# Performance work log

Measured on AMD Instinct MI355X. Metric: run time of the kernel, lower is better.

Reference implementation:

```python
import jax, jax.numpy as jnp
import numpy as np

STRIDE = 1
PAD = 1
K = 3  # kernel is asserted 3x3 in the original module


def _conv2d(x, w, b):
    out = jax.lax.conv_general_dilated(
        x, w, (STRIDE, STRIDE), [(PAD, PAD), (PAD, PAD)],
        dimension_numbers=("NCHW", "OIHW", "NCHW"))
    return out + b[None, :, None, None]


def _bilinear_sample(img, py, px):
    # img: [C, H, W]; py, px: [9, Ho, Wo] float sampling coords.
    # Zero-padded bilinear sampling (matches torchvision deform_conv2d).
    H, W = img.shape[1], img.shape[2]
    y0f = jnp.floor(py)
    x0f = jnp.floor(px)
    ly = py - y0f
    lx = px - x0f
    y0 = y0f.astype(jnp.int32)
    x0 = x0f.astype(jnp.int32)

    def g(yi, xi):
        valid = ((yi >= 0) & (yi < H) & (xi >= 0) & (xi < W)).astype(img.dtype)
        v = img[:, jnp.clip(yi, 0, H - 1), jnp.clip(xi, 0, W - 1)]  # [C,9,Ho,Wo]
        return v * valid[None]

    v00 = g(y0, x0)
    v01 = g(y0, x0 + 1)
    v10 = g(y0 + 1, x0)
    v11 = g(y0 + 1, x0 + 1)
    return (v00 * (1 - ly) * (1 - lx) + v01 * (1 - ly) * lx
            + v10 * ly * (1 - lx) + v11 * ly * lx)  # [C,9,Ho,Wo]


def setup_inputs() -> dict:
    key = jax.random.key(0)
    k1, k2, k3, k4 = jax.random.split(key, 4)
    B, C_in, C_out, H, W = 8, 64, 64, 128, 128
    x = jax.random.normal(k1, (B, C_in, H, W), dtype=jnp.float32)
    # offset predictor params (zero-init in original; small random here so
    # offsets are non-trivial, ~1-2 px)
    offset_w = jax.random.normal(k2, (4, C_in, K, K), dtype=jnp.float32) * 0.05
    offset_b = jax.random.normal(k3, (4,), dtype=jnp.float32) * 0.05
    weight = jax.random.normal(k4, (C_out, C_in, K, K), dtype=jnp.float32)
    return {"x": x, "offset_w": offset_w, "offset_b": offset_b, "weight": weight}


def reference(x, offset_w, offset_b, weight):
    B, C, H, W = x.shape
    o = _conv2d(x, offset_w, offset_b)  # [B, 4, Ho, Wo]
    o_t, o_b, o_l, o_r = o[:, 0], o[:, 1], o[:, 2], o[:, 3]
    z = jnp.zeros_like(o_t)
    # Original builds offset = cat([o_t,0,o_b]*3, [o_l]*3,[0]*3,[o_r]*3) (18 ch)
    # and torchvision reads interleaved (dy_k, dx_k) = (ch[2k], ch[2k+1]).
    # Faithful literal per-kernel-point offsets:
    dy = jnp.stack([o_t, o_b, z, o_t, o_b, o_l, z, z, o_r], axis=1)  # [B,9,Ho,Wo]
    dx = jnp.stack([z, o_t, o_b, z, o_l, o_l, z, o_r, o_r], axis=1)  # [B,9,Ho,Wo]
    Ho, Wo = o.shape[2], o.shape[3]
    ki = jnp.arange(9) // 3
    kj = jnp.arange(9) % 3
    base_y = (jnp.arange(Ho)[None, :, None] * STRIDE - PAD + ki[:, None, None])  # [9,Ho,1]
    base_x = (jnp.arange(Wo)[None, None, :] * STRIDE - PAD + kj[:, None, None])  # [9,1,Wo]
    py = base_y.astype(x.dtype) + dy  # [B,9,Ho,Wo]
    px = base_x.astype(x.dtype) + dx
    sampled = jax.vmap(_bilinear_sample)(x, py, px)  # [B,C,9,Ho,Wo]
    out = jnp.einsum("bckhw,ock->bohw", sampled,
                     weight.reshape(weight.shape[0], C, 9))
    return out
```

## Files before the change

### kernel.cpp

```cpp
#include <hip/hip_runtime.h>

#define H_   128
#define W_   128
#define CIN  64
#define COUT 64
#define B_   8
#define HW_  (H_*W_)

__global__ __launch_bounds__(256) void offsets_kernel(
    const float* __restrict__ x, const float* __restrict__ ow,
    const float* __restrict__ ob, float* __restrict__ o)
{
    __shared__ float xs[16][4][W_];
    __shared__ __align__(16) float wl[576][4];

    int tid = threadIdx.x;
    int blk = blockIdx.x;
    int b  = blk >> 6;
    int h0 = (blk & 63) << 1;

    for (int idx = tid; idx < 2304; idx += 256) {
        int ck = idx >> 2, j = idx & 3;
        int c = ck / 9, kk = ck - c * 9;
        wl[ck][j] = ow[(j * CIN + c) * 9 + kk];
    }

    float acc0 = 0.f, acc1 = 0.f, acc2 = 0.f, acc3 = 0.f;
    int hr = tid >> 7;
    int w  = tid & 127;

    for (int cc = 0; cc < 4; ++cc) {
        __syncthreads();
        for (int idx = tid; idx < 16 * 4 * W_; idx += 256) {
            int c_l = idx >> 9;
            int rem = idx & 511;
            int row = rem >> 7;
            int ww  = rem & 127;
            int gy  = h0 - 1 + row;
            float v = 0.f;
            if (gy >= 0 && gy < H_)
                v = x[((size_t)(b * CIN + cc * 16 + c_l) * H_ + gy) * W_ + ww];
            xs[c_l][row][ww] = v;
        }
        __syncthreads();
        for (int c_l = 0; c_l < 16; ++c_l) {
            int ckbase = (cc * 16 + c_l) * 9;
            #pragma unroll
            for (int ki = 0; ki < 3; ++ki) {
                #pragma unroll
                for (int kj = 0; kj < 3; ++kj) {
                    int wx = w - 1 + kj;
                    float v = (wx >= 0 && wx < W_) ? xs[c_l][hr + ki][wx] : 0.f;
                    float4 wv = *(const float4*)&wl[ckbase + ki * 3 + kj][0];
                    acc0 += v * wv.x; acc1 += v * wv.y;
                    acc2 += v * wv.z; acc3 += v * wv.w;
                }
            }
        }
    }

    int h = h0 + hr;
    size_t base = ((size_t)(b * 4) * H_ + h) * W_ + w;
    o[base]            = acc0 + ob[0];
    o[base + HW_]      = acc1 + ob[1];
    o[base + 2 * HW_]  = acc2 + ob[2];
    o[base + 3 * HW_]  = acc3 + ob[3];
}

__global__ void wtrans_kernel(const float* __restrict__ w, float* __restrict__ wT)
{
    int idx = blockIdx.x * 256 + threadIdx.x;
    if (idx < 576 * COUT) {
        int ck = idx >> 6, co = idx & 63;
        wT[idx] = w[co * 576 + ck];
    }
}

__global__ __launch_bounds__(256) void main_kernel(
    const float* __restrict__ x, const float* __restrict__ o,
    const float* __restrict__ wT, float* __restrict__ out)
{
    __shared__ __align__(16) int   aaddr[9][64][4];
    __shared__ __align__(16) float awt[9][64][4];
    __shared__ __align__(16) float s_lds[72 * 64];
    __shared__ __align__(16) float w_lds[72 * 64];

    int tid = threadIdx.x;
    int blk = blockIdx.x;
    int b   = blk >> 8;
    int rem = blk & 255;
    int h   = rem >> 1;
    int w0  = (rem & 1) << 6;

    for (int idx = tid; idx < 576; idx += 256) {
        int p = idx & 63;
        int k = idx >> 6;
        int w = w0 + p;
        size_t obase = ((size_t)(b * 4) * H_ + h) * W_ + w;
        float t  = o[obase];
        float bo = o[obase + HW_];
        float l  = o[obase + 2 * HW_];
        float r  = o[obase + 3 * HW_];
        float dy, dx;
        switch (k) {
            case 0: dy = t;   dx = 0.f; break;
            case 1: dy = bo;  dx = t;   break;
            case 2: dy = 0.f; dx = bo;  break;
            case 3: dy = t;   dx = 0.f; break;
            case 4: dy = bo;  dx = l;   break;
            case 5: dy = l;   dx = l;   break;
            case 6: dy = 0.f; dx = 0.f; break;
            case 7: dy = 0.f; dx = r;   break;
            default: dy = r;  dx = r;   break;
        }
        float py = (float)(h - 1 + k / 3) + dy;
        float px = (float)(w - 1 + (k % 3)) + dx;
        float y0f = floorf(py), x0f = floorf(px);
        float ly = py - y0f, lx = px - x0f;
        int y0 = (int)y0f, x0 = (int)x0f;
        int y1 = y0 + 1,   x1 = x0 + 1;
        bool vy0 = ((unsigned)y0 < (unsigned)H_);
        bool vy1 = ((unsigned)y1 < (unsigned)H_);
        bool vx0 = ((unsigned)x0 < (unsigned)W_);
        bool vx1 = ((unsigned)x1 < (unsigned)W_);
        int y0c = min(max(y0, 0), H_ - 1), y1c = min(max(y1, 0), H_ - 1);
        int x0c = min(max(x0, 0), W_ - 1), x1c = min(max(x1, 0), W_ - 1);
        aaddr[k][p][0] = y0c * W_ + x0c;
        aaddr[k][p][1] = y0c * W_ + x1c;
        aaddr[k][p][2] = y1c * W_ + x0c;
        aaddr[k][p][3] = y1c * W_ + x1c;
        float omly = 1.f - ly, omlx = 1.f - lx;
        awt[k][p][0] = (vy0 && vx0) ? omly * omlx : 0.f;
        awt[k][p][1] = (vy0 && vx1) ? omly * lx   : 0.f;
        awt[k][p][2] = (vy1 && vx0) ? ly * omlx   : 0.f;
        awt[k][p][3] = (vy1 && vx1) ? ly * lx     : 0.f;
    }
    __syncthreads();

    float acc[4][4] = {};
    int tp = tid & 15;
    int tc = tid >> 4;
    const float4* wT4 = (const float4*)wT;

    for (int cc = 0; cc < 8; ++cc) {
        for (int idx = tid; idx < 72 * 64; idx += 256) {
            int p = idx & 63;
            int r = idx >> 6;
            int k   = r % 9;
            int c_l = r / 9;
            int4   a4 = *(const int4*)&aaddr[k][p][0];
            float4 w4 = *(const float4*)&awt[k][p][0];
            const float* xb = x + ((size_t)(b * CIN + cc * 8 + c_l) << 14);
            float s = w4.x * xb[a4.x] + w4.y * xb[a4.y]
                    + w4.z * xb[a4.z] + w4.w * xb[a4.w];
            s_lds[idx] = s;
        }
        for (int idx = tid; idx < 1152; idx += 256) {
            ((float4*)w_lds)[idx] = wT4[cc * 1152 + idx];
        }
        __syncthreads();
        #pragma unroll 8
        for (int r = 0; r < 72; ++r) {
            float4 sv = *(const float4*)&s_lds[r * 64 + tp * 4];
            float4 wv = *(const float4*)&w_lds[r * 64 + tc * 4];
            float svv[4] = {sv.x, sv.y, sv.z, sv.w};
            float wvv[4] = {wv.x, wv.y, wv.z, wv.w};
            #pragma unroll
            for (int i = 0; i < 4; ++i)
                #pragma unroll
                for (int j = 0; j < 4; ++j)
                    acc[i][j] += svv[i] * wvv[j];
        }
        __syncthreads();
    }

    #pragma unroll
    for (int j = 0; j < 4; ++j) {
        int co = tc * 4 + j;
        size_t ob2 = ((size_t)(b * COUT + co) * H_ + h) * W_ + w0 + tp * 4;
        float4 v = make_float4(acc[0][j], acc[1][j], acc[2][j], acc[3][j]);
        *(float4*)&out[ob2] = v;
    }
}

extern "C" void kernel_launch(void* const* d_in, const int* in_sizes, int n_in,
                              void* d_out, int out_size, void* d_ws, size_t ws_size,
                              hipStream_t stream)
{
    const float* x  = (const float*)d_in[0];
    const float* ow = (const float*)d_in[1];
    const float* ob = (const float*)d_in[2];
    const float* wt = (const float*)d_in[3];
    float* out  = (float*)d_out;
    float* o_ws = (float*)d_ws;
    float* wT   = o_ws + (size_t)B_ * 4 * HW_;

    offsets_kernel<<<dim3(512), dim3(256), 0, stream>>>(x, ow, ob, o_ws);
    wtrans_kernel<<<dim3(144), dim3(256), 0, stream>>>(wt, wT);
    main_kernel<<<dim3(2048), dim3(256), 0, stream>>>(x, o_ws, wT, out);
}
```

Baseline: 434.4 us.

## Rewrite deformable conv main loop with bf16 MFMA and per-row blocks

Result: faster. 408.3 us (-6.0%).

```diff
diff --git a/kernel.cpp b/kernel.cpp
--- a/kernel.cpp
+++ b/kernel.cpp
@@ -7,116 +7,134 @@
 #define B_   8
 #define HW_  (H_*W_)
 
-__global__ __launch_bounds__(256) void offsets_kernel(
-    const float* __restrict__ x, const float* __restrict__ ow,
+typedef __attribute__((ext_vector_type(8))) short  short8;
+typedef __attribute__((ext_vector_type(8))) __bf16 bf16x8;
+typedef __attribute__((ext_vector_type(4))) float  f32x4;
+
+__device__ __forceinline__ ushort bf16r(float f) {
+    uint u = __builtin_bit_cast(uint, f);
+    u += 0x7fff + ((u >> 16) & 1);
+    return (ushort)(u >> 16);
+}
+
+__global__ void prep_kernel(const float* __restrict__ wt, const float* __restrict__ ow,
+                            float* __restrict__ owT, ushort* __restrict__ wTT2)
+{
+    int idx = blockIdx.x * 256 + threadIdx.x;
+    if (idx < 9 * 64 * 64) {
+        int kk = idx >> 12;
+        int r  = idx & 4095;
+        int co = r >> 6, c = r & 63;
+        wTT2[idx] = bf16r(wt[(co * 64 + c) * 9 + kk]);
+    }
+    if (idx < 576 * 4) {
+        int ck = idx >> 2, j = idx & 3;
+        owT[idx] = ow[j * 576 + ck];
+    }
+}
+
+__global__ __launch_bounds__(128) void offsets_kernel(
+    const float* __restrict__ x, const float* __restrict__ owT,
     const float* __restrict__ ob, float* __restrict__ o)
 {
-    __shared__ float xs[16][4][W_];
-    __shared__ __align__(16) float wl[576][4];
+    __shared__ float xs[16][3][132];
 
     int tid = threadIdx.x;
     int blk = blockIdx.x;
-    int b  = blk >> 6;
-    int h0 = (blk & 63) << 1;
-
-    for (int idx = tid; idx < 2304; idx += 256) {
-        int ck = idx >> 2, j = idx & 3;
-        int c = ck / 9, kk = ck - c * 9;
-        wl[ck][j] = ow[(j * CIN + c) * 9 + kk];
-    }
-
-    float acc0 = 0.f, acc1 = 0.f, acc2 = 0.f, acc3 = 0.f;
-    int hr = tid >> 7;
-    int w  = tid & 127;
+    int b = blk >> 7, h = blk & 127;
+    int w = tid;
+
+    for (int i = tid; i < 16 * 3; i += 128) {
+        int c = i / 3, r = i - c * 3;
+        xs[c][r][0] = 0.f; xs[c][r][1] = 0.f;
+        xs[c][r][130] = 0.f; xs[c][r][131] = 0.f;
+    }
+
+    float a0 = 0.f, a1 = 0.f, a2 = 0.f, a3 = 0.f;
+    const float4* owT4 = (const float4*)owT;
 
     for (int cc = 0; cc < 4; ++cc) {
         __syncthreads();
-        for (int idx = tid; idx < 16 * 4 * W_; idx += 256) {
-            int c_l = idx >> 9;
-            int rem = idx & 511;
-            int row = rem >> 7;
-            int ww  = rem & 127;
-            int gy  = h0 - 1 + row;
+        for (int idx = tid; idx < 16 * 3 * 128; idx += 128) {
+            int c_l = idx / 384;
+            int rem = idx - c_l * 384;
+            int row = rem >> 7, ww = rem & 127;
+            int gy = h - 1 + row;
             float v = 0.f;
-            if (gy >= 0 && gy < H_)
+            if ((unsigned)gy < (unsigned)H_)
                 v = x[((size_t)(b * CIN + cc * 16 + c_l) * H_ + gy) * W_ + ww];
-            xs[c_l][row][ww] = v;
-        }
-        __syncthreads();
+            xs[c_l][row][ww + 2] = v;
+        }
+        __syncthreads();
+        #pragma unroll
         for (int c_l = 0; c_l < 16; ++c_l) {
-            int ckbase = (cc * 16 + c_l) * 9;
+            int ckb = (cc * 16 + c_l) * 9;
             #pragma unroll
             for (int ki = 0; ki < 3; ++ki) {
                 #pragma unroll
                 for (int kj = 0; kj < 3; ++kj) {
-                    int wx = w - 1 + kj;
-                    float v = (wx >= 0 && wx < W_) ? xs[c_l][hr + ki][wx] : 0.f;
-                    float4 wv = *(const float4*)&wl[ckbase + ki * 3 + kj][0];
-                    acc0 += v * wv.x; acc1 += v * wv.y;
-                    acc2 += v * wv.z; acc3 += v * wv.w;
+                    float v = xs[c_l][ki][w + kj + 1];
+                    float4 wv = owT4[ckb + ki * 3 + kj];
+                    a0 += v * wv.x; a1 += v * wv.y;
+                    a2 += v * wv.z; a3 += v * wv.w;
                 }
             }
         }
     }
 
-    int h = h0 + hr;
     size_t base = ((size_t)(b * 4) * H_ + h) * W_ + w;
-    o[base]            = acc0 + ob[0];
-    o[base + HW_]      = acc1 + ob[1];
-    o[base + 2 * HW_]  = acc2 + ob[2];
-    o[base + 3 * HW_]  = acc3 + ob[3];
-}
-
-__global__ void wtrans_kernel(const float* __restrict__ w, float* __restrict__ wT)
-{
-    int idx = blockIdx.x * 256 + threadIdx.x;
-    if (idx < 576 * COUT) {
-        int ck = idx >> 6, co = idx & 63;
-        wT[idx] = w[co * 576 + ck];
-    }
-}
-
-__global__ __launch_bounds__(256) void main_kernel(
+    o[base]           = a0 + ob[0];
+    o[base + HW_]     = a1 + ob[1];
+    o[base + 2 * HW_] = a2 + ob[2];
+    o[base + 3 * HW_] = a3 + ob[3];
+}
+
+__global__ __launch_bounds__(128) void main_kernel(
     const float* __restrict__ x, const float* __restrict__ o,
-    const float* __restrict__ wT, float* __restrict__ out)
-{
-    __shared__ __align__(16) int   aaddr[9][64][4];
-    __shared__ __align__(16) float awt[9][64][4];
-    __shared__ __align__(16) float s_lds[72 * 64];
-    __shared__ __align__(16) float w_lds[72 * 64];
-
-    int tid = threadIdx.x;
-    int blk = blockIdx.x;
-    int b   = blk >> 8;
-    int rem = blk & 255;
-    int h   = rem >> 1;
-    int w0  = (rem & 1) << 6;
-
-    for (int idx = tid; idx < 576; idx += 256) {
-        int p = idx & 63;
-        int k = idx >> 6;
-        int w = w0 + p;
-        size_t obase = ((size_t)(b * 4) * H_ + h) * W_ + w;
-        float t  = o[obase];
-        float bo = o[obase + HW_];
-        float l  = o[obase + 2 * HW_];
-        float r  = o[obase + 3 * HW_];
+    const ushort* __restrict__ wTT2, float* __restrict__ out)
+{
+    __shared__ ushort a_lds[128][72];
+    __shared__ ushort w_lds[64][72];
+
+    int tid  = threadIdx.x;
+    int blk  = blockIdx.x;
+    int b    = blk >> 7, h = blk & 127;
+    int w    = tid;
+    int lane = tid & 63, wid = tid >> 6;
+
+    size_t obase = ((size_t)(b * 4) * H_ + h) * W_ + w;
+    float t  = o[obase];
+    float bo = o[obase + HW_];
+    float l_ = o[obase + 2 * HW_];
+    float r_ = o[obase + 3 * HW_];
+
+    const float* xb = x + ((size_t)b * CIN * HW_);
+
+    f32x4 zero4 = {0.f, 0.f, 0.f, 0.f};
+    f32x4 acc[4][4];
+    #pragma unroll
+    for (int i = 0; i < 4; ++i)
+        #pragma unroll
+        for (int j = 0; j < 4; ++j) acc[i][j] = zero4;
+
+    for (int cc = 0; cc < 9; ++cc) {
         float dy, dx;
-        switch (k) {
+        switch (cc) {
             case 0: dy = t;   dx = 0.f; break;
             case 1: dy = bo;  dx = t;   break;
             case 2: dy = 0.f; dx = bo;  break;
             case 3: dy = t;   dx = 0.f; break;
-            case 4: dy = bo;  dx = l;   break;
-            case 5: dy = l;   dx = l;   break;
+            case 4: dy = bo;  dx = l_;  break;
+            case 5: dy = l_;  dx = l_;  break;
             case 6: dy = 0.f; dx = 0.f; break;
-            case 7: dy = 0.f; dx = r;   break;
-            default: dy = r;  dx = r;   break;
-        }
-        float py = (float)(h - 1 + k / 3) + dy;
-        float px = (float)(w - 1 + (k % 3)) + dx;
-        float y0f = floorf(py), x0f = floorf(px);
-        float ly = py - y0f, lx = px - x0f;
+            case 7: dy = 0.f; dx = r_;  break;
+            default: dy = r_; dx = r_;  break;
+        }
+        int ki = cc / 3, kj = cc - ki * 3;
+        float py  = (float)(h - 1 + ki) + dy;
+        float pxf = (float)(w - 1 + kj) + dx;
+        float y0f = floorf(py), x0f = floorf(pxf);
+        float ly = py - y0f, lx = pxf - x0f;
         int y0 = (int)y0f, x0 = (int)x0f;
         int y1 = y0 + 1,   x1 = x0 + 1;
         bool vy0 = ((unsigned)y0 < (unsigned)H_);
@@ -125,61 +143,71 @@
         bool vx1 = ((unsigned)x1 < (unsigned)W_);
         int y0c = min(max(y0, 0), H_ - 1), y1c = min(max(y1, 0), H_ - 1);
         int x0c = min(max(x0, 0), W_ - 1), x1c = min(max(x1, 0), W_ - 1);
-        aaddr[k][p][0] = y0c * W_ + x0c;
-        aaddr[k][p][1] = y0c * W_ + x1c;
-        aaddr[k][p][2] = y1c * W_ + x0c;
-        aaddr[k][p][3] = y1c * W_ + x1c;
+        int ia0 = y0c * W_ + x0c, ia1 = y0c * W_ + x1c;
+        int ia2 = y1c * W_ + x0c, ia3 = y1c * W_ + x1c;
         float omly = 1.f - ly, omlx = 1.f - lx;
-        awt[k][p][0] = (vy0 && vx0) ? omly * omlx : 0.f;
-        awt[k][p][1] = (vy0 && vx1) ? omly * lx   : 0.f;
-        awt[k][p][2] = (vy1 && vx0) ? ly * omlx   : 0.f;
-        awt[k][p][3] = (vy1 && vx1) ? ly * lx     : 0.f;
-    }
-    __syncthreads();
-
-    float acc[4][4] = {};
-    int tp = tid & 15;
-    int tc = tid >> 4;
-    const float4* wT4 = (const float4*)wT;
-
-    for (int cc = 0; cc < 8; ++cc) {
-        for (int idx = tid; idx < 72 * 64; idx += 256) {
-            int p = idx & 63;
-            int r = idx >> 6;
-            int k   = r % 9;
-            int c_l = r / 9;
-            int4   a4 = *(const int4*)&aaddr[k][p][0];
-            float4 w4 = *(const float4*)&awt[k][p][0];
-            const float* xb = x + ((size_t)(b * CIN + cc * 8 + c_l) << 14);
-            float s = w4.x * xb[a4.x] + w4.y * xb[a4.y]
-                    + w4.z * xb[a4.z] + w4.w * xb[a4.w];
-            s_lds[idx] = s;
-        }
-        for (int idx = tid; idx < 1152; idx += 256) {
-            ((float4*)w_lds)[idx] = wT4[cc * 1152 + idx];
-        }
-        __syncthreads();
-        #pragma unroll 8
-        for (int r = 0; r < 72; ++r) {
-            float4 sv = *(const float4*)&s_lds[r * 64 + tp * 4];
-            float4 wv = *(const float4*)&w_lds[r * 64 + tc * 4];
-            float svv[4] = {sv.x, sv.y, sv.z, sv.w};
-            float wvv[4] = {wv.x, wv.y, wv.z, wv.w};
+        float wt0 = (vy0 && vx0) ? omly * omlx : 0.f;
+        float wt1 = (vy0 && vx1) ? omly * lx   : 0.f;
+        float wt2 = (vy1 && vx0) ? ly * omlx   : 0.f;
+        float wt3 = (vy1 && vx1) ? ly * lx     : 0.f;
+
+        #pragma unroll
+        for (int c8 = 0; c8 < 8; ++c8) {
+            uint pk[4];
+            #pragma unroll
+            for (int i2 = 0; i2 < 4; ++i2) {
+                const float* xc0 = xb + ((size_t)(c8 * 8 + i2 * 2) << 14);
+                const float* xc1 = xb + ((size_t)(c8 * 8 + i2 * 2 + 1) << 14);
+                float s0 = wt0 * xc0[ia0] + wt1 * xc0[ia1]
+                         + wt2 * xc0[ia2] + wt3 * xc0[ia3];
+                float s1 = wt0 * xc1[ia0] + wt1 * xc1[ia1]
+                         + wt2 * xc1[ia2] + wt3 * xc1[ia3];
+                pk[i2] = (uint)bf16r(s0) | ((uint)bf16r(s1) << 16);
+            }
+            *(uint4*)&a_lds[tid][c8 * 8] = make_uint4(pk[0], pk[1], pk[2], pk[3]);
+        }
+
+        {
+            const uint4* src = (const uint4*)(wTT2 + cc * 4096);
+            #pragma unroll
+            for (int q = 0; q < 4; ++q) {
+                int idx = tid + q * 128;
+                int co = idx >> 3, c0 = (idx & 7) * 8;
+                *(uint4*)&w_lds[co][c0] = src[idx];
+            }
+        }
+        __syncthreads();
+
+        #pragma unroll
+        for (int s = 0; s < 2; ++s) {
+            int krow = s * 32 + (lane >> 4) * 8;
+            bf16x8 af[4];
             #pragma unroll
             for (int i = 0; i < 4; ++i)
+                af[i] = __builtin_bit_cast(bf16x8,
+                    *(const short8*)&a_lds[wid * 64 + i * 16 + (lane & 15)][krow]);
+            #pragma unroll
+            for (int j = 0; j < 4; ++j) {
+                bf16x8 bf = __builtin_bit_cast(bf16x8,
+                    *(const short8*)&w_lds[j * 16 + (lane & 15)][krow]);
                 #pragma unroll
-                for (int j = 0; j < 4; ++j)
-                    acc[i][j] += svv[i] * wvv[j];
+                for (int i = 0; i < 4; ++i)
+                    acc[i][j] = __builtin_amdgcn_mfma_f32_16x16x32_bf16(
+                        af[i], bf, acc[i][j], 0, 0, 0);
+            }
         }
         __syncthreads();
     }
 
     #pragma unroll
-    for (int j = 0; j < 4; ++j) {
-        int co = tc * 4 + j;
-        size_t ob2 = ((size_t)(b * COUT + co) * H_ + h) * W_ + w0 + tp * 4;
-        float4 v = make_float4(acc[0][j], acc[1][j], acc[2][j], acc[3][j]);
-        *(float4*)&out[ob2] = v;
+    for (int i = 0; i < 4; ++i) {
+        int pr = wid * 64 + i * 16 + (lane >> 4) * 4;
+        #pragma unroll
+        for (int j = 0; j < 4; ++j) {
+            int co = j * 16 + (lane & 15);
+            *(float4*)&out[((size_t)(b * COUT + co) * H_ + h) * W_ + pr] =
+                *(float4*)&acc[i][j];
+        }
     }
 }
 
@@ -191,11 +219,13 @@
     const float* ow = (const float*)d_in[1];
     const float* ob = (const float*)d_in[2];
     const float* wt = (const float*)d_in[3];
-    float* out  = (float*)d_out;
-    float* o_ws = (float*)d_ws;
-    float* wT   = o_ws + (size_t)B_ * 4 * HW_;
-
-    offsets_kernel<<<dim3(512), dim3(256), 0, stream>>>(x, ow, ob, o_ws);
-    wtrans_kernel<<<dim3(144), dim3(256), 0, stream>>>(wt, wT);
-    main_kernel<<<dim3(2048), dim3(256), 0, stream>>>(x, o_ws, wT, out);
-}
+    float* out = (float*)d_out;
+
+    float*  o_ws = (float*)d_ws;
+    float*  owT  = o_ws + (size_t)B_ * 4 * HW_;
+    ushort* wTT2 = (ushort*)(owT + 2304);
+
+    prep_kernel<<<dim3(144), dim3(256), 0, stream>>>(wt, ow, owT, wTT2);
+    offsets_kernel<<<dim3(1024), dim3(128), 0, stream>>>(x, owT, ob, o_ws);
+    main_kernel<<<dim3(1024), dim3(128), 0, stream>>>(x, o_ws, wTT2, out);
+}
```
